# Kernel tuning notes

Hardware: AMD Instinct MI355X
Metric: run time of the kernel (lower is better)

Reference implementation:

```python
import jax, jax.numpy as jnp
import numpy as np

B, N, D_IN, D_OUT, L, T = 8, 512, 1024, 1024, 16, 4096


def setup_inputs() -> dict:
    key = jax.random.key(0)
    k1, k2, k3 = jax.random.split(key, 3)
    pooled_vectors = jax.random.normal(k1, (B, N, D_IN), dtype=jnp.float32)
    # stacked nn.Linear weights, each (out, in), bias=False
    W = jax.random.normal(k2, (L, D_OUT, D_IN), dtype=jnp.float32) * 0.02
    pooling_indices = jnp.sort(jax.random.randint(k3, (N,), 0, T, dtype=jnp.int64))
    return {
        "pooled_vectors": pooled_vectors,
        "W": W,
        "pooling_indices": pooling_indices,
        "target_length": T,
    }


def reference(pooled_vectors, W, pooling_indices, target_length):
    # pooled_vectors: (B, N, D_in); W: (L, D_out, D_in); pooling_indices: (N,) sorted
    Bn, Nn, _ = pooled_vectors.shape
    Ln = W.shape[0]
    t = jnp.arange(target_length)
    # segment i covers [start_i, idx_i + 1); searchsorted finds the covering segment
    seg = jnp.searchsorted(pooling_indices, t, side="left")  # (T,)
    valid = seg < Nn  # positions past the last pooling index stay zero
    segc = jnp.clip(seg, 0, Nn - 1)
    start = jnp.where(segc > 0, pooling_indices[segc - 1] + 1, 0)
    lidx = jnp.minimum(t - start, Ln - 1)  # position-specific linear index, capped
    # apply all L position linears to every pooled vector: (B, N, L, D_out)
    trans = jnp.einsum("bnd,lod->bnlo", pooled_vectors, W)
    out = trans[:, segc, lidx]  # gather per output position -> (B, T, D_out)
    return jnp.where(valid[None, :, None], out, jnp.zeros((), out.dtype))
```

## Files before the change

### kernel.cpp

```cpp
#include <hip/hip_runtime.h>
#include <stdint.h>

#define B_    8
#define N_    512
#define DIN   1024
#define DOUT  1024
#define L_    16
#define T_    4096

#define BM 128
#define BN 128
#define BK 32
#define NB (DOUT / BN)
#define NKT (DIN / BK)
#define MT_MAX 288
#define ZROW ((long)B_ * N_)

typedef __attribute__((ext_vector_type(8))) short short8;
typedef __attribute__((ext_vector_type(4))) float f32x4;

#define POOLED_ELEMS ((long)B_ * N_ * DIN + DIN)
#define WS_W_OFF     ((size_t)POOLED_ELEMS * 2)
#define WS_META_OFF  (WS_W_OFF + (size_t)L_ * DOUT * DIN * 2)

__device__ __forceinline__ unsigned short f2bf(float f) {
  unsigned u = __float_as_uint(f);
  u += 0x7FFFu + ((u >> 16) & 1u);
  return (unsigned short)(u >> 16);
}

__device__ __forceinline__ void gload_lds16(const void* g, void* l) {
  __builtin_amdgcn_global_load_lds(
      (const __attribute__((address_space(1))) void*)g,
      (__attribute__((address_space(3))) void*)l, 16, 0, 0);
}

__device__ __forceinline__ void bar() {
  asm volatile("" ::: "memory");
  __builtin_amdgcn_s_barrier();
  asm volatile("" ::: "memory");
}

__global__ void k_convert(const float* __restrict__ pooled,
                          const float* __restrict__ W,
                          unsigned short* __restrict__ wsP,
                          unsigned short* __restrict__ wsW) {
  const long np4 = (long)B_ * N_ * DIN / 4;
  const long nw4 = (long)L_ * DOUT * DIN / 4;
  const long nz4 = DIN / 4;
  long i = (long)blockIdx.x * blockDim.x + threadIdx.x;
  const long stride = (long)gridDim.x * blockDim.x;
  for (; i < np4 + nw4 + nz4; i += stride) {
    if (i < np4) {
      float4 v = ((const float4*)pooled)[i];
      ushort4 o = { f2bf(v.x), f2bf(v.y), f2bf(v.z), f2bf(v.w) };
      ((ushort4*)wsP)[i] = o;
    } else if (i < np4 + nw4) {
      float4 v = ((const float4*)W)[i - np4];
      ushort4 o = { f2bf(v.x), f2bf(v.y), f2bf(v.z), f2bf(v.w) };
      ((ushort4*)wsW)[i - np4] = o;
    } else {
      ushort4 z = {0, 0, 0, 0};
      ((ushort4*)wsP)[i - nw4] = z;
    }
  }
}

__global__ void k_prep(const int* __restrict__ pidx,
                       unsigned* __restrict__ tlist,
                       int* __restrict__ goff, int* __restrict__ grows,
                       unsigned* __restrict__ table, int* __restrict__ ntiles) {
  __shared__ int sp[N_];
  __shared__ int cnt[L_], pos[L_];
  const int tid = threadIdx.x;
  if (tid < N_) sp[tid] = pidx[tid];
  if (tid < L_) cnt[tid] = 0;
  __syncthreads();

  int start = tid ? sp[tid - 1] + 1 : 0;
  int len = sp[tid] - start + 1;
  if (len < 0) len = 0;
  const int nfull = len < 15 ? len : 15;

  for (int l2 = 0; l2 < nfull; ++l2) atomicAdd(&cnt[l2], 1);
  if (len > 15) atomicAdd(&cnt[15], (len - 15 + 254) / 255);
  if (tid == N_ - 1) {
    int invlen = T_ - 1 - sp[N_ - 1];
    if (invlen > 0) atomicAdd(&cnt[15], (invlen + 254) / 255);
  }
  __syncthreads();
  if (tid == 0) {
    int off = 0;
    for (int l2 = 0; l2 < L_; ++l2) {
      pos[l2] = off; goff[l2] = off; grows[l2] = cnt[l2] * B_;
      off += cnt[l2];
    }
  }
  __syncthreads();

  for (int l2 = 0; l2 < nfull; ++l2) {
    int p = atomicAdd(&pos[l2], 1);
    tlist[p] = (unsigned)(start + l2) | ((unsigned)tid << 12) | (1u << 22);
  }
  if (len > 15) {
    int rem = len - 15, tt2 = start + 15;
    while (rem > 0) {
      int rr = rem > 255 ? 255 : rem;
      int p = atomicAdd(&pos[15], 1);
      tlist[p] = (unsigned)tt2 | ((unsigned)tid << 12) | ((unsigned)rr << 22);
      tt2 += rr; rem -= rr;
    }
  }
  if (tid == N_ - 1) {
    int tt2 = sp[N_ - 1] + 1;
    int rem = T_ - tt2;
    while (rem > 0) {
      int rr = rem > 255 ? 255 : rem;
      int p = atomicAdd(&pos[15], 1);
      tlist[p] = (unsigned)tt2 | (1023u << 12) | ((unsigned)rr << 22);
      tt2 += rr; rem -= rr;
    }
  }
  __syncthreads();
  if (tid == 0) {
    int tt = 0;
    for (int l2 = 0; l2 < L_; ++l2) {
      int rows = cnt[l2] * B_;
      for (int r0 = 0; r0 < rows; r0 += BM) table[tt++] = (unsigned)l2 | ((unsigned)r0 << 4);
    }
    *ntiles = tt;
  }
}

__global__ __launch_bounds__(256, 3)
void k_gemm(const unsigned short* __restrict__ wsP,
            const unsigned short* __restrict__ wsW,
            const unsigned* __restrict__ tlist,
            const int* __restrict__ goff,
            const int* __restrict__ grows,
            const unsigned* __restrict__ table,
            const int* __restrict__ ntiles,
            float* __restrict__ out) {
  const int bid = blockIdx.x;
  const int mt = bid >> 3;
  const int nt = bid & 7;
  if (mt >= *ntiles) return;

  const unsigned te = table[mt];
  const int l    = te & 15;
  const int row0 = (int)(te >> 4);
  const int toff = goff[l];
  const int rows = grows[l];

  __shared__ __align__(16) unsigned short As[3][BM * BK];
  __shared__ __align__(16) unsigned short Bs[3][BN * BK];

  const int tid  = threadIdx.x;
  const int lane = tid & 63;
  const int w    = tid >> 6;
  const int wm   = w >> 1;
  const int wn   = w & 1;

  const int srow = tid >> 2;
  const int sx4  = ((tid & 3) ^ ((srow >> 1) & 3)) * 16;
  const char* aptr0;
  const char* aptr1;
  {
    long re[2];
#pragma unroll
    for (int r = 0; r < 2; ++r) {
      int rg = row0 + r * 64 + srow;
      if (rg < rows) {
        unsigned e = tlist[toff + (rg >> 3)];
        unsigned n = (e >> 12) & 0x3FF;
        int b = rg & 7;
        re[r] = (n >= N_) ? ZROW * (long)DIN
                          : ((long)(b * N_ + (int)n)) * DIN;
      } else re[r] = ZROW * (long)DIN;
    }
    aptr0 = (const char*)(wsP + re[0]) + sx4;
    aptr1 = (const char*)(wsP + re[1]) + sx4;
  }
  const char* bptr0 = (const char*)(wsW + ((long)l * DOUT + nt * BN + srow) * DIN) + sx4;
  const char* bptr1 = (const char*)(wsW + ((long)l * DOUT + nt * BN + 64 + srow) * DIN) + sx4;

#define STG(t_, sb) do { \
  gload_lds16(aptr0 + (t_) * 64, (char*)As[sb] + w * 1024); \
  gload_lds16(aptr1 + (t_) * 64, (char*)As[sb] + 4096 + w * 1024); \
  gload_lds16(bptr0 + (t_) * 64, (char*)Bs[sb] + w * 1024); \
  gload_lds16(bptr1 + (t_) * 64, (char*)Bs[sb] + 4096 + w * 1024); } while (0)

  const int arow = wm * 64 + (lane & 15);
  const int brow = wn * 64 + (lane & 15);
  const int axr  = ((lane >> 4) ^ (((lane & 15) >> 1) & 3)) * 16;

  f32x4 acc[4][4];
#pragma unroll
  for (int m = 0; m < 4; ++m)
#pragma unroll
    for (int n = 0; n < 4; ++n)
      acc[m][n] = (f32x4){0.f, 0.f, 0.f, 0.f};

  short8 af[4], bf[4];

#define PHASE(t_, bb, sb) do { \
  const int t2_ = (t_) + 2; \
  if (t2_ < NKT) STG(t2_, sb); \
  _Pragma("unroll") for (int m_ = 0; m_ < 4; ++m_) \
    af[m_] = *(const short8*)((const char*)As[bb] + (arow + m_ * 16) * 64 + axr); \
  _Pragma("unroll") for (int n_ = 0; n_ < 4; ++n_) \
    bf[n_] = *(const short8*)((const char*)Bs[bb] + (brow + n_ * 16) * 64 + axr); \
  bar(); \
  asm volatile("s_waitcnt lgkmcnt(0)" ::: "memory"); \
  __builtin_amdgcn_s_setprio(1); \
  _Pragma("unroll") for (int n_ = 0; n_ < 4; ++n_) \
    _Pragma("unroll") for (int m_ = 0; m_ < 4; ++m_) \
      acc[m_][n_] = __builtin_amdgcn_mfma_f32_16x16x32_bf16(af[m_], bf[n_], acc[m_][n_], 0, 0, 0); \
  __builtin_amdgcn_s_setprio(0); \
  if (t2_ < NKT) asm volatile("s_waitcnt vmcnt(4)" ::: "memory"); \
  else           asm volatile("s_waitcnt vmcnt(0)" ::: "memory"); \
  bar(); \
} while (0)

  STG(0, 0);
  STG(1, 1);
  asm volatile("s_waitcnt vmcnt(4)" ::: "memory");
  bar();

  for (int j = 0; j < 11; ++j) {
    const int t0 = 3 * j;
    if (t0     < NKT) PHASE(t0,     0, 2);
    if (t0 + 1 < NKT) PHASE(t0 + 1, 1, 0);
    if (t0 + 2 < NKT) PHASE(t0 + 2, 2, 1);
  }

#pragma unroll
  for (int m = 0; m < 4; ++m) {
#pragma unroll
    for (int jj = 0; jj < 4; ++jj) {
      int rt = wm * 64 + m * 16 + (lane >> 4) * 4 + jj;
      int rg = row0 + rt;
      if (rg >= rows) continue;
      unsigned e = tlist[toff + (rg >> 3)];
      int b = rg & 7;
      int t0 = (int)(e & 0xFFFu);
      int rep = (int)(e >> 22);
      float* orow = out + ((long)b * T_ + t0) * DOUT + nt * BN + wn * 64 + (lane & 15);
      for (int r = 0; r < rep; ++r) {
#pragma unroll
        for (int n = 0; n < 4; ++n)
          orow[n * 16] = acc[m][n][jj];
        orow += DOUT;
      }
    }
  }
#undef STG
#undef PHASE
}

extern "C" void kernel_launch(void* const* d_in, const int* in_sizes, int n_in,
                              void* d_out, int out_size, void* d_ws, size_t ws_size,
                              hipStream_t stream) {
  const float* pooled = (const float*)d_in[0];
  const float* W      = (const float*)d_in[1];
  const int*   pidx   = (const int*)d_in[2];
  float* out = (float*)d_out;

  char* ws = (char*)d_ws;
  unsigned short* wsP = (unsigned short*)(ws);
  unsigned short* wsW = (unsigned short*)(ws + WS_W_OFF);
  int* meta  = (int*)(ws + WS_META_OFF);
  unsigned* tlist = (unsigned*)meta;
  int* goff  = meta + 8 * T_;
  int* grows = meta + 8 * T_ + 16;
  unsigned* table = (unsigned*)(meta + 8 * T_ + 32);
  int* ntiles = meta + 8 * T_ + 32 + MT_MAX;

  k_prep<<<1, 512, 0, stream>>>(pidx, tlist, goff, grows, table, ntiles);
  k_convert<<<2048, 256, 0, stream>>>(pooled, W, wsP, wsW);
  k_gemm<<<MT_MAX * NB, 256, 0, stream>>>(wsP, wsW, tlist, goff, grows, table,
                                          ntiles, out);
}
```

Measured before the change: 134.6 us.

## Make GEMM persistent with atomic tile queue and cross-tile prefetch pipeline

Replaces the one-block-per-tile grid with a fixed grid of 512 persistent blocks. Each block pulls M-tiles from a per-N-column atomic counter and prefetches the next tile's first K-stages during the tail of the current tile, using a 4-deep LDS ring instead of 3. This is meant to remove per-block launch and prologue/epilogue bubbles and improve load balance. In exchange it doubles LDS use, lowers launch bounds to 2 blocks per CU, and raises MT_MAX.

```diff
diff --git a/kernel.cpp b/kernel.cpp
--- a/kernel.cpp
+++ b/kernel.cpp
@@ -13,8 +13,9 @@
 #define BK 32
 #define NB (DOUT / BN)
 #define NKT (DIN / BK)
-#define MT_MAX 288
+#define MT_MAX 320
 #define ZROW ((long)B_ * N_)
+#define GRID_GEMM 512
 
 typedef __attribute__((ext_vector_type(8))) short short8;
 typedef __attribute__((ext_vector_type(4))) float f32x4;
@@ -69,12 +70,14 @@
 __global__ void k_prep(const int* __restrict__ pidx,
                        unsigned* __restrict__ tlist,
                        int* __restrict__ goff, int* __restrict__ grows,
-                       unsigned* __restrict__ table, int* __restrict__ ntiles) {
+                       unsigned* __restrict__ table, int* __restrict__ ntiles,
+                       int* __restrict__ ctr) {
   __shared__ int sp[N_];
   __shared__ int cnt[L_], pos[L_];
   const int tid = threadIdx.x;
   if (tid < N_) sp[tid] = pidx[tid];
   if (tid < L_) cnt[tid] = 0;
+  if (tid < 8) ctr[tid] = 0;
   __syncthreads();
 
   int start = tid ? sp[tid - 1] + 1 : 0;
@@ -132,7 +135,7 @@
   }
 }
 
-__global__ __launch_bounds__(256, 3)
+__global__ __launch_bounds__(256, 2)
 void k_gemm(const unsigned short* __restrict__ wsP,
             const unsigned short* __restrict__ wsW,
             const unsigned* __restrict__ tlist,
@@ -140,20 +143,14 @@
             const int* __restrict__ grows,
             const unsigned* __restrict__ table,
             const int* __restrict__ ntiles,
+            int* __restrict__ ctr,
             float* __restrict__ out) {
-  const int bid = blockIdx.x;
-  const int mt = bid >> 3;
-  const int nt = bid & 7;
-  if (mt >= *ntiles) return;
-
-  const unsigned te = table[mt];
-  const int l    = te & 15;
-  const int row0 = (int)(te >> 4);
-  const int toff = goff[l];
-  const int rows = grows[l];
-
-  __shared__ __align__(16) unsigned short As[3][BM * BK];
-  __shared__ __align__(16) unsigned short Bs[3][BN * BK];
+  const int nt = blockIdx.x & 7;
+  const int NT = *ntiles;
+
+  __shared__ __align__(16) unsigned short As[4][BM * BK];
+  __shared__ __align__(16) unsigned short Bs[4][BN * BK];
+  __shared__ int s_g;
 
   const int tid  = threadIdx.x;
   const int lane = tid & 63;
@@ -163,99 +160,134 @@
 
   const int srow = tid >> 2;
   const int sx4  = ((tid & 3) ^ ((srow >> 1) & 3)) * 16;
-  const char* aptr0;
-  const char* aptr1;
-  {
-    long re[2];
-#pragma unroll
-    for (int r = 0; r < 2; ++r) {
-      int rg = row0 + r * 64 + srow;
-      if (rg < rows) {
-        unsigned e = tlist[toff + (rg >> 3)];
-        unsigned n = (e >> 12) & 0x3FF;
-        int b = rg & 7;
-        re[r] = (n >= N_) ? ZROW * (long)DIN
-                          : ((long)(b * N_ + (int)n)) * DIN;
-      } else re[r] = ZROW * (long)DIN;
-    }
-    aptr0 = (const char*)(wsP + re[0]) + sx4;
-    aptr1 = (const char*)(wsP + re[1]) + sx4;
-  }
-  const char* bptr0 = (const char*)(wsW + ((long)l * DOUT + nt * BN + srow) * DIN) + sx4;
-  const char* bptr1 = (const char*)(wsW + ((long)l * DOUT + nt * BN + 64 + srow) * DIN) + sx4;
-
-#define STG(t_, sb) do { \
-  gload_lds16(aptr0 + (t_) * 64, (char*)As[sb] + w * 1024); \
-  gload_lds16(aptr1 + (t_) * 64, (char*)As[sb] + 4096 + w * 1024); \
-  gload_lds16(bptr0 + (t_) * 64, (char*)Bs[sb] + w * 1024); \
-  gload_lds16(bptr1 + (t_) * 64, (char*)Bs[sb] + 4096 + w * 1024); } while (0)
+
+  if (tid == 0) s_g = atomicAdd(&ctr[nt], 1);
+  __syncthreads();
+  int mt = s_g;
+  if (mt >= NT) return;
+
+#define MKPTRS(mtv, A0, A1, B0, B1, TOFF, ROW0, ROWS) do {                    \
+    unsigned tev = table[mtv];                                                \
+    int lv = tev & 15; (ROW0) = (int)(tev >> 4);                              \
+    (TOFF) = goff[lv]; (ROWS) = grows[lv];                                    \
+    long re0, re1;                                                            \
+    { int rg = (ROW0) + srow;                                                 \
+      if (rg < (ROWS)) { unsigned e = tlist[(TOFF) + (rg >> 3)];              \
+        unsigned n = (e >> 12) & 0x3FF; int b = rg & 7;                       \
+        re0 = (n >= N_) ? ZROW * (long)DIN : ((long)(b * N_ + (int)n)) * DIN; \
+      } else re0 = ZROW * (long)DIN; }                                        \
+    { int rg = (ROW0) + 64 + srow;                                            \
+      if (rg < (ROWS)) { unsigned e = tlist[(TOFF) + (rg >> 3)];              \
+        unsigned n = (e >> 12) & 0x3FF; int b = rg & 7;                       \
+        re1 = (n >= N_) ? ZROW * (long)DIN : ((long)(b * N_ + (int)n)) * DIN; \
+      } else re1 = ZROW * (long)DIN; }                                        \
+    (A0) = (const char*)(wsP + re0) + sx4;                                    \
+    (A1) = (const char*)(wsP + re1) + sx4;                                    \
+    (B0) = (const char*)(wsW + ((long)lv * DOUT + nt * BN + srow) * DIN) + sx4;       \
+    (B1) = (const char*)(wsW + ((long)lv * DOUT + nt * BN + 64 + srow) * DIN) + sx4;  \
+  } while (0)
+
+  const char *a0c, *a1c, *b0c, *b1c;
+  const char *a0n, *a1n, *b0n, *b1n;
+  int toff_c, row0_c, rows_c;
+  int toff_n = 0, row0_n = 0, rows_n = 0;
+  MKPTRS(mt, a0c, a1c, b0c, b1c, toff_c, row0_c, rows_c);
+  a0n = a0c; a1n = a1c; b0n = b0c; b1n = b1c;
+
+#define STG_C(kt_, sb) do { \
+  gload_lds16(a0c + (kt_) * 64, (char*)As[sb] + w * 1024); \
+  gload_lds16(a1c + (kt_) * 64, (char*)As[sb] + 4096 + w * 1024); \
+  gload_lds16(b0c + (kt_) * 64, (char*)Bs[sb] + w * 1024); \
+  gload_lds16(b1c + (kt_) * 64, (char*)Bs[sb] + 4096 + w * 1024); } while (0)
+#define STG_N(kt_, sb) do { \
+  gload_lds16(a0n + (kt_) * 64, (char*)As[sb] + w * 1024); \
+  gload_lds16(a1n + (kt_) * 64, (char*)As[sb] + 4096 + w * 1024); \
+  gload_lds16(b0n + (kt_) * 64, (char*)Bs[sb] + w * 1024); \
+  gload_lds16(b1n + (kt_) * 64, (char*)Bs[sb] + 4096 + w * 1024); } while (0)
 
   const int arow = wm * 64 + (lane & 15);
   const int brow = wn * 64 + (lane & 15);
   const int axr  = ((lane >> 4) ^ (((lane & 15) >> 1) & 3)) * 16;
 
   f32x4 acc[4][4];
-#pragma unroll
-  for (int m = 0; m < 4; ++m)
-#pragma unroll
-    for (int n = 0; n < 4; ++n)
-      acc[m][n] = (f32x4){0.f, 0.f, 0.f, 0.f};
-
   short8 af[4], bf[4];
 
-#define PHASE(t_, bb, sb) do { \
-  const int t2_ = (t_) + 2; \
-  if (t2_ < NKT) STG(t2_, sb); \
-  _Pragma("unroll") for (int m_ = 0; m_ < 4; ++m_) \
-    af[m_] = *(const short8*)((const char*)As[bb] + (arow + m_ * 16) * 64 + axr); \
-  _Pragma("unroll") for (int n_ = 0; n_ < 4; ++n_) \
-    bf[n_] = *(const short8*)((const char*)Bs[bb] + (brow + n_ * 16) * 64 + axr); \
-  bar(); \
-  asm volatile("s_waitcnt lgkmcnt(0)" ::: "memory"); \
-  __builtin_amdgcn_s_setprio(1); \
-  _Pragma("unroll") for (int n_ = 0; n_ < 4; ++n_) \
-    _Pragma("unroll") for (int m_ = 0; m_ < 4; ++m_) \
-      acc[m_][n_] = __builtin_amdgcn_mfma_f32_16x16x32_bf16(af[m_], bf[n_], acc[m_][n_], 0, 0, 0); \
-  __builtin_amdgcn_s_setprio(0); \
-  if (t2_ < NKT) asm volatile("s_waitcnt vmcnt(4)" ::: "memory"); \
-  else           asm volatile("s_waitcnt vmcnt(0)" ::: "memory"); \
-  bar(); \
-} while (0)
-
-  STG(0, 0);
-  STG(1, 1);
-  asm volatile("s_waitcnt vmcnt(4)" ::: "memory");
+#define VM(n_) asm volatile("s_waitcnt vmcnt(" #n_ ")" ::: "memory")
+#define PH(T) do {                                                            \
+    if ((T) < NKT - 3)      STG_C((T) + 3, ((T) + 3) & 3);                    \
+    else if (has)           STG_N((T) - (NKT - 3), ((T) + 3) & 3);            \
+    _Pragma("unroll") for (int m_ = 0; m_ < 4; ++m_)                          \
+      af[m_] = *(const short8*)((const char*)As[(T) & 3] + (arow + m_ * 16) * 64 + axr); \
+    _Pragma("unroll") for (int n_ = 0; n_ < 4; ++n_)                          \
+      bf[n_] = *(const short8*)((const char*)Bs[(T) & 3] + (brow + n_ * 16) * 64 + axr); \
+    bar();                                                                    \
+    asm volatile("s_waitcnt lgkmcnt(0)" ::: "memory");                        \
+    __builtin_amdgcn_s_setprio(1);                                            \
+    _Pragma("unroll") for (int n_ = 0; n_ < 4; ++n_)                          \
+      _Pragma("unroll") for (int m_ = 0; m_ < 4; ++m_)                        \
+        acc[m_][n_] = __builtin_amdgcn_mfma_f32_16x16x32_bf16(af[m_], bf[n_], acc[m_][n_], 0, 0, 0); \
+    __builtin_amdgcn_s_setprio(0);                                            \
+    if ((T) < NKT - 3 || has) { VM(8); }                                      \
+    else if ((T) == NKT - 3)  { VM(4); }                                      \
+    else if ((T) == NKT - 2)  { VM(0); }                                      \
+    bar();                                                                    \
+  } while (0)
+
+  STG_C(0, 0); STG_C(1, 1); STG_C(2, 2);
+  VM(8);
   bar();
 
-  for (int j = 0; j < 11; ++j) {
-    const int t0 = 3 * j;
-    if (t0     < NKT) PHASE(t0,     0, 2);
-    if (t0 + 1 < NKT) PHASE(t0 + 1, 1, 0);
-    if (t0 + 2 < NKT) PHASE(t0 + 2, 2, 1);
-  }
-
-#pragma unroll
-  for (int m = 0; m < 4; ++m) {
-#pragma unroll
-    for (int jj = 0; jj < 4; ++jj) {
-      int rt = wm * 64 + m * 16 + (lane >> 4) * 4 + jj;
-      int rg = row0 + rt;
-      if (rg >= rows) continue;
-      unsigned e = tlist[toff + (rg >> 3)];
-      int b = rg & 7;
-      int t0 = (int)(e & 0xFFFu);
-      int rep = (int)(e >> 22);
-      float* orow = out + ((long)b * T_ + t0) * DOUT + nt * BN + wn * 64 + (lane & 15);
-      for (int r = 0; r < rep; ++r) {
-#pragma unroll
-        for (int n = 0; n < 4; ++n)
-          orow[n * 16] = acc[m][n][jj];
-        orow += DOUT;
+  for (;;) {
+    if (tid == 0) s_g = atomicAdd(&ctr[nt], 1);
+    bool has = false;
+
+#pragma unroll
+    for (int m = 0; m < 4; ++m)
+#pragma unroll
+      for (int n = 0; n < 4; ++n)
+        acc[m][n] = (f32x4){0.f, 0.f, 0.f, 0.f};
+
+    PH(0); PH(1); PH(2); PH(3); PH(4);
+    {
+      int mtn = s_g;
+      has = (mtn < NT);
+      if (has) MKPTRS(mtn, a0n, a1n, b0n, b1n, toff_n, row0_n, rows_n);
+    }
+    PH(5);  PH(6);  PH(7);  PH(8);  PH(9);  PH(10); PH(11); PH(12);
+    PH(13); PH(14); PH(15); PH(16); PH(17); PH(18); PH(19); PH(20);
+    PH(21); PH(22); PH(23); PH(24); PH(25); PH(26); PH(27); PH(28);
+    PH(29); PH(30); PH(31);
+
+#pragma unroll
+    for (int m = 0; m < 4; ++m) {
+#pragma unroll
+      for (int jj = 0; jj < 4; ++jj) {
+        int rt = wm * 64 + m * 16 + (lane >> 4) * 4 + jj;
+        int rg = row0_c + rt;
+        if (rg >= rows_c) continue;
+        unsigned e = tlist[toff_c + (rg >> 3)];
+        int b = rg & 7;
+        int t0 = (int)(e & 0xFFFu);
+        int rep = (int)(e >> 22);
+        float* orow = out + ((long)b * T_ + t0) * DOUT + nt * BN + wn * 64 + (lane & 15);
+        for (int r = 0; r < rep; ++r) {
+#pragma unroll
+          for (int n = 0; n < 4; ++n)
+            orow[n * 16] = acc[m][n][jj];
+          orow += DOUT;
+        }
       }
     }
-  }
-#undef STG
-#undef PHASE
+
+    if (!has) break;
+    a0c = a0n; a1c = a1n; b0c = b0n; b1c = b1n;
+    toff_c = toff_n; row0_c = row0_n; rows_c = rows_n;
+  }
+#undef PH
+#undef VM
+#undef STG_C
+#undef STG_N
+#undef MKPTRS
 }
 
 extern "C" void kernel_launch(void* const* d_in, const int* in_sizes, int n_in,
@@ -275,9 +307,10 @@
   int* grows = meta + 8 * T_ + 16;
   unsigned* table = (unsigned*)(meta + 8 * T_ + 32);
   int* ntiles = meta + 8 * T_ + 32 + MT_MAX;
-
-  k_prep<<<1, 512, 0, stream>>>(pidx, tlist, goff, grows, table, ntiles);
+  int* ctr    = ntiles + 1;
+
+  k_prep<<<1, 512, 0, stream>>>(pidx, tlist, goff, grows, table, ntiles, ctr);
   k_convert<<<2048, 256, 0, stream>>>(pooled, W, wsP, wsW);
-  k_gemm<<<MT_MAX * NB, 256, 0, stream>>>(wsP, wsW, tlist, goff, grows, table,
-                                          ntiles, out);
-}
+  k_gemm<<<GRID_GEMM, 256, 0, stream>>>(wsP, wsW, tlist, goff, grows, table,
+                                        ntiles, ctr, out);
+}
```

After: 150.4 us. 11.8% more time.

## Pre-pack weights into MFMA fragment layout and load B directly to registers

Applied to the files above, without the earlier changes.

The convert kernel now writes the bf16 weights in a fragment-packed layout, so each lane's 8-element MFMA B operand is contiguous. The GEMM loads B fragments straight from global memory into registers, skipping the LDS staging. The A operand keeps LDS staging but moves from a 3-stage to a 2-stage buffer, and the custom barriers become __syncthreads. This cuts LDS traffic and footprint. In exchange it relies on global-to-register latency being hidden by register double-buffering, and each wave re-fetches B from L2 instead of sharing it through LDS.

```diff
diff --git a/kernel.cpp b/kernel.cpp
--- a/kernel.cpp
+++ b/kernel.cpp
@@ -35,33 +35,37 @@
       (__attribute__((address_space(3))) void*)l, 16, 0, 0);
 }
 
-__device__ __forceinline__ void bar() {
-  asm volatile("" ::: "memory");
-  __builtin_amdgcn_s_barrier();
-  asm volatile("" ::: "memory");
-}
-
 __global__ void k_convert(const float* __restrict__ pooled,
                           const float* __restrict__ W,
                           unsigned short* __restrict__ wsP,
-                          unsigned short* __restrict__ wsW) {
+                          unsigned short* __restrict__ wsW2) {
   const long np4 = (long)B_ * N_ * DIN / 4;
-  const long nw4 = (long)L_ * DOUT * DIN / 4;
   const long nz4 = DIN / 4;
+  const long nwu = (long)L_ * 64 * 32 * 64;
   long i = (long)blockIdx.x * blockDim.x + threadIdx.x;
   const long stride = (long)gridDim.x * blockDim.x;
-  for (; i < np4 + nw4 + nz4; i += stride) {
+  for (; i < np4 + nz4 + nwu; i += stride) {
     if (i < np4) {
       float4 v = ((const float4*)pooled)[i];
       ushort4 o = { f2bf(v.x), f2bf(v.y), f2bf(v.z), f2bf(v.w) };
       ((ushort4*)wsP)[i] = o;
-    } else if (i < np4 + nw4) {
-      float4 v = ((const float4*)W)[i - np4];
-      ushort4 o = { f2bf(v.x), f2bf(v.y), f2bf(v.z), f2bf(v.w) };
-      ((ushort4*)wsW)[i - np4] = o;
+    } else if (i < np4 + nz4) {
+      ushort4 z = {0, 0, 0, 0};
+      ((ushort4*)wsP)[i] = z;
     } else {
-      ushort4 z = {0, 0, 0, 0};
-      ((ushort4*)wsP)[i - nw4] = z;
+      long u = i - np4 - nz4;
+      int ln = (int)(u & 63); long tmp = u >> 6;
+      int kb = (int)(tmp & 31); tmp >>= 5;
+      int cb = (int)(tmp & 63); int l = (int)(tmp >> 6);
+      int r = cb * 16 + (ln & 15);
+      int k = kb * 32 + (ln >> 4) * 8;
+      const float* src = W + ((long)l * DOUT + r) * DIN + k;
+      float4 v0 = *(const float4*)(src);
+      float4 v1 = *(const float4*)(src + 4);
+      ushort4 o0 = { f2bf(v0.x), f2bf(v0.y), f2bf(v0.z), f2bf(v0.w) };
+      ushort4 o1 = { f2bf(v1.x), f2bf(v1.y), f2bf(v1.z), f2bf(v1.w) };
+      ((ushort4*)wsW2)[u * 2]     = o0;
+      ((ushort4*)wsW2)[u * 2 + 1] = o1;
     }
   }
 }
@@ -134,7 +138,7 @@
 
 __global__ __launch_bounds__(256, 3)
 void k_gemm(const unsigned short* __restrict__ wsP,
-            const unsigned short* __restrict__ wsW,
+            const unsigned short* __restrict__ wsW2,
             const unsigned* __restrict__ tlist,
             const int* __restrict__ goff,
             const int* __restrict__ grows,
@@ -152,8 +156,7 @@
   const int toff = goff[l];
   const int rows = grows[l];
 
-  __shared__ __align__(16) unsigned short As[3][BM * BK];
-  __shared__ __align__(16) unsigned short Bs[3][BN * BK];
+  __shared__ __align__(16) unsigned short As[2][BM * BK];
 
   const int tid  = threadIdx.x;
   const int lane = tid & 63;
@@ -181,57 +184,56 @@
     aptr0 = (const char*)(wsP + re[0]) + sx4;
     aptr1 = (const char*)(wsP + re[1]) + sx4;
   }
-  const char* bptr0 = (const char*)(wsW + ((long)l * DOUT + nt * BN + srow) * DIN) + sx4;
-  const char* bptr1 = (const char*)(wsW + ((long)l * DOUT + nt * BN + 64 + srow) * DIN) + sx4;
-
-#define STG(t_, sb) do { \
+
+#define STG_A(t_, sb) do { \
   gload_lds16(aptr0 + (t_) * 64, (char*)As[sb] + w * 1024); \
-  gload_lds16(aptr1 + (t_) * 64, (char*)As[sb] + 4096 + w * 1024); \
-  gload_lds16(bptr0 + (t_) * 64, (char*)Bs[sb] + w * 1024); \
-  gload_lds16(bptr1 + (t_) * 64, (char*)Bs[sb] + 4096 + w * 1024); } while (0)
+  gload_lds16(aptr1 + (t_) * 64, (char*)As[sb] + 4096 + w * 1024); } while (0)
 
   const int arow = wm * 64 + (lane & 15);
-  const int brow = wn * 64 + (lane & 15);
   const int axr  = ((lane >> 4) ^ (((lane & 15) >> 1) & 3)) * 16;
 
-  f32x4 acc[4][4];
-#pragma unroll
-  for (int m = 0; m < 4; ++m)
-#pragma unroll
-    for (int n = 0; n < 4; ++n)
-      acc[m][n] = (f32x4){0.f, 0.f, 0.f, 0.f};
-
-  short8 af[4], bf[4];
-
-#define PHASE(t_, bb, sb) do { \
-  const int t2_ = (t_) + 2; \
-  if (t2_ < NKT) STG(t2_, sb); \
-  _Pragma("unroll") for (int m_ = 0; m_ < 4; ++m_) \
-    af[m_] = *(const short8*)((const char*)As[bb] + (arow + m_ * 16) * 64 + axr); \
-  _Pragma("unroll") for (int n_ = 0; n_ < 4; ++n_) \
-    bf[n_] = *(const short8*)((const char*)Bs[bb] + (brow + n_ * 16) * 64 + axr); \
-  bar(); \
-  asm volatile("s_waitcnt lgkmcnt(0)" ::: "memory"); \
+  const unsigned short* wbase =
+      wsW2 + (((long)l * 64 + nt * 8 + wn * 4) * 32) * 512 + lane * 8;
+#define LDB(dst, t_) do { _Pragma("unroll") \
+  for (int n_ = 0; n_ < 4; ++n_) \
+    dst[n_] = *(const short8*)(wbase + n_ * (32 * 512) + (t_) * 512); } while (0)
+
+#define DSA(bb) do { _Pragma("unroll") \
+  for (int m_ = 0; m_ < 4; ++m_) \
+    af[m_] = *(const short8*)((const char*)As[bb] + (arow + m_ * 16) * 64 + axr); } while (0)
+
+#define MM(BF) do { \
   __builtin_amdgcn_s_setprio(1); \
   _Pragma("unroll") for (int n_ = 0; n_ < 4; ++n_) \
     _Pragma("unroll") for (int m_ = 0; m_ < 4; ++m_) \
-      acc[m_][n_] = __builtin_amdgcn_mfma_f32_16x16x32_bf16(af[m_], bf[n_], acc[m_][n_], 0, 0, 0); \
-  __builtin_amdgcn_s_setprio(0); \
-  if (t2_ < NKT) asm volatile("s_waitcnt vmcnt(4)" ::: "memory"); \
-  else           asm volatile("s_waitcnt vmcnt(0)" ::: "memory"); \
-  bar(); \
-} while (0)
-
-  STG(0, 0);
-  STG(1, 1);
-  asm volatile("s_waitcnt vmcnt(4)" ::: "memory");
-  bar();
-
-  for (int j = 0; j < 11; ++j) {
-    const int t0 = 3 * j;
-    if (t0     < NKT) PHASE(t0,     0, 2);
-    if (t0 + 1 < NKT) PHASE(t0 + 1, 1, 0);
-    if (t0 + 2 < NKT) PHASE(t0 + 2, 2, 1);
+      acc[m_][n_] = __builtin_amdgcn_mfma_f32_16x16x32_bf16(af[m_], BF[n_], acc[m_][n_], 0, 0, 0); \
+  __builtin_amdgcn_s_setprio(0); } while (0)
+
+  f32x4 acc[4][4];
+#pragma unroll
+  for (int m = 0; m < 4; ++m)
+#pragma unroll
+    for (int n = 0; n < 4; ++n)
+      acc[m][n] = (f32x4){0.f, 0.f, 0.f, 0.f};
+
+  short8 af[4], bf_a[4], bf_b[4];
+
+  STG_A(0, 0);
+  LDB(bf_a, 0);
+  __syncthreads();
+
+#pragma unroll
+  for (int j = 0; j < NKT / 2; ++j) {
+    const int t0 = 2 * j, t1 = 2 * j + 1;
+    STG_A(t1, 1);
+    LDB(bf_b, t1);
+    DSA(0);
+    MM(bf_a);
+    __syncthreads();
+    if (t0 + 2 < NKT) { STG_A(t0 + 2, 0); LDB(bf_a, t0 + 2); }
+    DSA(1);
+    MM(bf_b);
+    __syncthreads();
   }
 
 #pragma unroll
@@ -254,8 +256,10 @@
       }
     }
   }
-#undef STG
-#undef PHASE
+#undef STG_A
+#undef LDB
+#undef DSA
+#undef MM
 }
 
 extern "C" void kernel_launch(void* const* d_in, const int* in_sizes, int n_in,
@@ -267,8 +271,8 @@
   float* out = (float*)d_out;
 
   char* ws = (char*)d_ws;
-  unsigned short* wsP = (unsigned short*)(ws);
-  unsigned short* wsW = (unsigned short*)(ws + WS_W_OFF);
+  unsigned short* wsP  = (unsigned short*)(ws);
+  unsigned short* wsW2 = (unsigned short*)(ws + WS_W_OFF);
   int* meta  = (int*)(ws + WS_META_OFF);
   unsigned* tlist = (unsigned*)meta;
   int* goff  = meta + 8 * T_;
@@ -277,7 +281,7 @@
   int* ntiles = meta + 8 * T_ + 32 + MT_MAX;
 
   k_prep<<<1, 512, 0, stream>>>(pidx, tlist, goff, grows, table, ntiles);
-  k_convert<<<2048, 256, 0, stream>>>(pooled, W, wsP, wsW);
-  k_gemm<<<MT_MAX * NB, 256, 0, stream>>>(wsP, wsW, tlist, goff, grows, table,
+  k_convert<<<2048, 256, 0, stream>>>(pooled, W, wsP, wsW2);
+  k_gemm<<<MT_MAX * NB, 256, 0, stream>>>(wsP, wsW2, tlist, goff, grows, table,
                                           ntiles, out);
 }
```

Measured after the change: 130.2 us. -3.3%, faster.
